# Kernel optimization log

Hardware: AMD Instinct MI355X
Metric: run time of the kernel (lower is better)

The kernel has to match this reference:

```python
import jax, jax.numpy as jnp
import numpy as np

BETA = 0.25
EPS = 1e-10


def setup_inputs() -> dict:
    key = jax.random.key(0)
    k1, k2 = jax.random.split(key)
    z = jax.random.normal(k1, (16, 256, 32, 32), dtype=jnp.float32)
    # Original init: uniform(-1/n_embed, 1/n_embed)
    n_embed, embed_dim = 8192, 256
    codebook = jax.random.uniform(k2, (n_embed, embed_dim), dtype=jnp.float32,
                                  minval=-1.0 / n_embed, maxval=1.0 / n_embed)
    return {"z": z, "codebook": codebook}


def reference(z, codebook):
    B, C, H, W = z.shape
    n_embed = codebook.shape[0]
    zp = jnp.transpose(z, (0, 2, 3, 1))            # (B,H,W,C)
    zf = zp.reshape(-1, C)                          # (N,C)
    # squared L2 distances (N, n_embed)
    d = (jnp.sum(zf * zf, axis=1, keepdims=True)
         + jnp.sum(codebook * codebook, axis=1)
         - 2.0 * zf @ codebook.T)
    idx = jnp.argmin(d, axis=1)                     # (N,)
    zq = codebook[idx].reshape(zp.shape)            # gather == one-hot @ codebook
    commitment_loss = jnp.mean((jax.lax.stop_gradient(zq) - zp) ** 2)
    embedding_loss = jnp.mean((zq - jax.lax.stop_gradient(zp)) ** 2)
    loss = embedding_loss + BETA * commitment_loss
    # straight-through estimator
    zq_st = zp + jax.lax.stop_gradient(zq - zp)
    # perplexity from mean one-hot usage (counts / N)
    counts = jnp.zeros((n_embed,), dtype=zf.dtype).at[idx].add(1.0)
    avg_probs = counts / zf.shape[0]
    perplexity = jnp.exp(-jnp.sum(avg_probs * jnp.log(avg_probs + EPS)))
    zq_out = jnp.transpose(zq_st, (0, 3, 1, 2))     # (B,C,H,W)
    return zq_out, loss, perplexity, idx
```

## Files before the change

kernel.cpp:

```cpp
#include <hip/hip_runtime.h>
#include <math.h>

#define Nrows 16384
#define NE 8192
#define Kdim 256
#define HWsz 1024
#define BETAF 0.25f

typedef __attribute__((ext_vector_type(8))) short bf16x8;
typedef __attribute__((ext_vector_type(16))) float f32x16;
typedef unsigned short u16;

__device__ inline u16 bf16_rne(float x) {
  unsigned int u = __float_as_uint(x);
  return (u16)((u + 0x7FFFu + ((u >> 16) & 1u)) >> 16);
}
__device__ inline float bf16_tof(u16 h) {
  return __uint_as_float(((unsigned int)h) << 16);
}
__device__ inline void gll16(const void* g, void* l) {
  __builtin_amdgcn_global_load_lds(
      (const __attribute__((address_space(1))) unsigned int*)g,
      (__attribute__((address_space(3))) unsigned int*)l, 16, 0, 0);
}

__global__ __launch_bounds__(256) void cc_kernel(const float* __restrict__ cb,
                                                 float* __restrict__ cc) {
  int wave = threadIdx.x >> 6;
  int lane = threadIdx.x & 63;
  int row = blockIdx.x * 4 + wave;
  const float4 v = *(const float4*)(cb + (size_t)row * Kdim + lane * 4);
  float s = v.x * v.x + v.y * v.y + v.z * v.z + v.w * v.w;
  for (int off = 32; off; off >>= 1) s += __shfl_down(s, off);
  if (lane == 0) cc[row] = s;
}

__global__ __launch_bounds__(256) void conv_cb(const float* __restrict__ cb,
                                               u16* __restrict__ Cf) {
  const int g = blockIdx.x * 256 + threadIdx.x;
  const int j = g >> 4, k16 = g & 15;
  const float* src = cb + (size_t)j * Kdim + k16 * 16;
  float f[16];
#pragma unroll
  for (int q = 0; q < 4; ++q) {
    const float4 v = ((const float4*)src)[q];
    f[q * 4 + 0] = v.x; f[q * 4 + 1] = v.y; f[q * 4 + 2] = v.z; f[q * 4 + 3] = v.w;
  }
  u16 h[3][16];
#pragma unroll
  for (int i = 0; i < 16; ++i) {
    const u16 q0 = bf16_rne(f[i]);
    const float r1 = f[i] - bf16_tof(q0);
    const u16 q1 = bf16_rne(r1);
    const float r2 = r1 - bf16_tof(q1);
    h[0][i] = q0; h[1][i] = q1; h[2][i] = bf16_rne(r2);
  }
  const int j32 = j >> 5, li = j & 31;
#pragma unroll
  for (int arr = 0; arr < 3; ++arr) {
#pragma unroll
    for (int kh = 0; kh < 2; ++kh) {
      const size_t off = ((size_t)(j32 * 3 + arr) * 16 + k16) * 512 + (kh * 32 + li) * 8;
      *(int4*)(Cf + off) = *(int4*)&h[arr][kh * 8];
    }
  }
}

__global__ __launch_bounds__(256) void conv_z(const float* __restrict__ z,
                                              u16* __restrict__ Zf,
                                              float* __restrict__ zz) {
  __shared__ float tile[64][68];
  const int t = threadIdx.x;
  const int bid = blockIdx.x;
  const int n0 = bid * 64;
  const int b = bid >> 4;
  const int hw0 = (bid & 15) << 6;
  const float* zb = z + (size_t)b * (Kdim * HWsz) + hw0;
  float zzacc = 0.f;
  const int rr = t >> 2;
  const int kq = (t & 3) * 16;
  for (int kc = 0; kc < 4; ++kc) {
#pragma unroll
    for (int i = 0; i < 16; ++i) {
      const int idx = i * 256 + t;
      const int k = idx >> 6, r = idx & 63;
      tile[r][k] = zb[(size_t)(kc * 64 + k) * HWsz + r];
    }
    __syncthreads();
    if (t < 64) {
      for (int k = 0; k < 64; ++k) {
        const float a = tile[t][k];
        zzacc = fmaf(a, a, zzacc);
      }
    }
    u16 h[3][16];
#pragma unroll
    for (int i = 0; i < 16; ++i) {
      const float fv = tile[rr][kq + i];
      const u16 q0 = bf16_rne(fv);
      const float r1 = fv - bf16_tof(q0);
      const u16 q1 = bf16_rne(r1);
      const float r2 = r1 - bf16_tof(q1);
      h[0][i] = q0; h[1][i] = q1; h[2][i] = bf16_rne(r2);
    }
    const int k16 = kc * 4 + (t & 3);
    const int n32 = bid * 2 + (rr >> 5), li = rr & 31;
#pragma unroll
    for (int arr = 0; arr < 3; ++arr) {
#pragma unroll
      for (int kh = 0; kh < 2; ++kh) {
        const size_t off = ((size_t)(n32 * 3 + arr) * 16 + k16) * 512 + (kh * 32 + li) * 8;
        *(int4*)(Zf + off) = *(int4*)&h[arr][kh * 8];
      }
    }
    __syncthreads();
  }
  if (t < 64) zz[n0 + t] = zzacc;
}

__global__ __launch_bounds__(1024) void vq_gemm(
    const u16* __restrict__ Cf, const u16* __restrict__ Zf,
    const float* __restrict__ cc, const float* __restrict__ zz,
    float* __restrict__ pd, int* __restrict__ pj) {
  __shared__ u16 Zl[49152];
  __shared__ float ccs[1024];
  __shared__ float redD[16][64];
  __shared__ int redJ[16][64];

  const int t = threadIdx.x;
  const int lane = t & 63;
  const int w = __builtin_amdgcn_readfirstlane(t >> 6);
  const int bid = blockIdx.x;
  const int ctg = bid & 7;
  const int rt = bid >> 3;

  ccs[t] = cc[ctg * 1024 + t];

  float zzv[2];
  zzv[0] = zz[rt * 64 + (lane & 31)];
  zzv[1] = zz[rt * 64 + 32 + (lane & 31)];

#pragma unroll
  for (int i = 0; i < 6; ++i) {
    const int g = w * 6 + i;
    const int rg = g & 1, k16 = (g >> 1) & 15, arr = g >> 5;
    gll16(Zf + ((size_t)((rt * 2 + rg) * 3 + arr) * 16 + k16) * 512 + lane * 8,
          &Zl[g * 512]);
  }
  __syncthreads();

  const f32x16 zero16 = {0,0,0,0,0,0,0,0,0,0,0,0,0,0,0,0};
  f32x16 acc[2][2];
  acc[0][0] = zero16; acc[0][1] = zero16; acc[1][0] = zero16; acc[1][1] = zero16;

  for (int ch = 0; ch < 16; ++ch) {
    bf16x8 af[3][2], bfr[3][2];
#pragma unroll
    for (int arr = 0; arr < 3; ++arr) {
#pragma unroll
      for (int x = 0; x < 2; ++x) {
        af[arr][x] = *(const bf16x8*)(
            Cf + ((size_t)((ctg * 32 + w * 2 + x) * 3 + arr) * 16 + ch) * 512 + lane * 8);
        bfr[arr][x] = *(const bf16x8*)&Zl[((arr * 16 + ch) * 2 + x) * 512 + lane * 8];
      }
    }
#define PROD(pa, pb) \
  acc[0][0] = __builtin_amdgcn_mfma_f32_32x32x16_bf16(af[pa][0], bfr[pb][0], acc[0][0], 0, 0, 0); \
  acc[0][1] = __builtin_amdgcn_mfma_f32_32x32x16_bf16(af[pa][0], bfr[pb][1], acc[0][1], 0, 0, 0); \
  acc[1][0] = __builtin_amdgcn_mfma_f32_32x32x16_bf16(af[pa][1], bfr[pb][0], acc[1][0], 0, 0, 0); \
  acc[1][1] = __builtin_amdgcn_mfma_f32_32x32x16_bf16(af[pa][1], bfr[pb][1], acc[1][1], 0, 0, 0);
    PROD(0, 0) PROD(0, 1) PROD(1, 0) PROD(1, 1) PROD(0, 2) PROD(2, 0)
#undef PROD
  }

  float bd[2] = {INFINITY, INFINITY};
  int bj[2] = {0, 0};
#pragma unroll
  for (int ci = 0; ci < 2; ++ci) {
#pragma unroll
    for (int ri = 0; ri < 2; ++ri) {
#pragma unroll
      for (int reg = 0; reg < 16; ++reg) {
        const int cl = w * 64 + ci * 32 +
                       (reg & 3) + ((reg >> 2) * 8) + ((lane >> 5) * 4);
        const float d = (zzv[ri] + ccs[cl]) - 2.0f * acc[ci][ri][reg];
        const int j = ctg * 1024 + cl;
        if (d < bd[ri]) { bd[ri] = d; bj[ri] = j; }
      }
    }
  }

#pragma unroll
  for (int ri = 0; ri < 2; ++ri) {
    const float od = __shfl_xor(bd[ri], 32);
    const int oj = __shfl_xor(bj[ri], 32);
    if (od < bd[ri] || (od == bd[ri] && oj < bj[ri])) { bd[ri] = od; bj[ri] = oj; }
  }
  if (lane < 32) {
    redD[w][lane] = bd[0]; redJ[w][lane] = bj[0];
    redD[w][32 + lane] = bd[1]; redJ[w][32 + lane] = bj[1];
  }
  __syncthreads();
  if (t < 64) {
    float d0 = redD[0][t];
    int j0 = redJ[0][t];
#pragma unroll
    for (int x = 1; x < 16; ++x) {
      const float d = redD[x][t];
      const int j = redJ[x][t];
      if (d < d0 || (d == d0 && j < j0)) { d0 = d; j0 = j; }
    }
    const int n = rt * 64 + t;
    pd[(size_t)ctg * Nrows + n] = d0;
    pj[(size_t)ctg * Nrows + n] = j0;
  }
}

__global__ __launch_bounds__(256) void vq_combine(const float* __restrict__ pd,
                                                  const int* __restrict__ pj,
                                                  int* __restrict__ idx_int,
                                                  float* __restrict__ out_idxf,
                                                  int* __restrict__ counts) {
  const int n = blockIdx.x * 256 + threadIdx.x;
  float d0 = pd[n];
  int j0 = pj[n];
  for (int s = 1; s < 8; ++s) {
    const float d = pd[(size_t)s * Nrows + n];
    const int j = pj[(size_t)s * Nrows + n];
    if (d < d0 || (d == d0 && j < j0)) { d0 = d; j0 = j; }
  }
  idx_int[n] = j0;
  out_idxf[n] = (float)j0;
  atomicAdd(&counts[j0], 1);
}

__global__ __launch_bounds__(256) void vq_gather_loss(
    const float* __restrict__ z, const float* __restrict__ cb,
    const int* __restrict__ idx_int, float* __restrict__ outz,
    float* __restrict__ loss_sum) {
  const int g = blockIdx.x * 256 + threadIdx.x;
  const int hw4 = g & 255;
  const int c = (g >> 8) & 255;
  const int b = g >> 16;
  const int n = b * HWsz + hw4 * 4;
  const float4 zv = *(const float4*)(z + (size_t)g * 4);
  const int4 j4 = *(const int4*)(idx_int + n);
  float4 q;
  q.x = cb[(size_t)j4.x * Kdim + c];
  q.y = cb[(size_t)j4.y * Kdim + c];
  q.z = cb[(size_t)j4.z * Kdim + c];
  q.w = cb[(size_t)j4.w * Kdim + c];
  *(float4*)(outz + (size_t)g * 4) = q;
  float dx = q.x - zv.x, dy = q.y - zv.y, dz = q.z - zv.z, dw = q.w - zv.w;
  float s = dx * dx + dy * dy + dz * dz + dw * dw;
  for (int off = 32; off; off >>= 1) s += __shfl_down(s, off);
  __shared__ float ws4[4];
  if ((threadIdx.x & 63) == 0) ws4[threadIdx.x >> 6] = s;
  __syncthreads();
  if (threadIdx.x == 0) atomicAdd(loss_sum, (ws4[0] + ws4[1]) + (ws4[2] + ws4[3]));
}

__global__ __launch_bounds__(256) void vq_final(const int* __restrict__ counts,
                                                const float* __restrict__ loss_sum,
                                                float* __restrict__ out_sc) {
  float h = 0.f;
  for (int i = threadIdx.x; i < NE; i += 256) {
    float p = (float)counts[i] * (1.0f / 16384.0f);
    h += p * logf(p + 1e-10f);
  }
  for (int off = 32; off; off >>= 1) h += __shfl_down(h, off);
  __shared__ float hs[4];
  if ((threadIdx.x & 63) == 0) hs[threadIdx.x >> 6] = h;
  __syncthreads();
  if (threadIdx.x == 0) {
    float H = (hs[0] + hs[1]) + (hs[2] + hs[3]);
    float m = loss_sum[0] * (1.0f / 4194304.0f);
    out_sc[0] = m + BETAF * m;
    out_sc[1] = expf(-H);
  }
}

extern "C" void kernel_launch(void* const* d_in, const int* in_sizes, int n_in,
                              void* d_out, int out_size, void* d_ws, size_t ws_size,
                              hipStream_t stream) {
  const float* z = (const float*)d_in[0];
  const float* cb = (const float*)d_in[1];
  float* out = (float*)d_out;
  float* out_zq = out;
  float* out_sc = out + 4194304;
  float* out_idx = out + 4194306;

  char* wp = (char*)d_ws;
  u16* Cf = (u16*)wp;           wp += (size_t)NE * Kdim * 2 * 3;
  u16* Zf = (u16*)wp;           wp += (size_t)Nrows * Kdim * 2 * 3;
  float* cc = (float*)wp;       wp += (size_t)NE * 4;
  float* zz = (float*)wp;       wp += (size_t)Nrows * 4;
  float* pd = (float*)wp;       wp += (size_t)8 * Nrows * 4;
  int* pj = (int*)wp;           wp += (size_t)8 * Nrows * 4;
  int* idx_int = (int*)wp;      wp += (size_t)Nrows * 4;
  int* counts = (int*)wp;       wp += (size_t)NE * 4;
  float* loss_sum = (float*)wp; wp += 64;

  hipMemsetAsync(counts, 0, (size_t)NE * 4, stream);
  hipMemsetAsync(loss_sum, 0, 4, stream);

  cc_kernel<<<NE / 4, 256, 0, stream>>>(cb, cc);
  conv_cb<<<NE * 16 / 256, 256, 0, stream>>>(cb, Cf);
  conv_z<<<Nrows / 64, 256, 0, stream>>>(z, Zf, zz);
  vq_gemm<<<2048, 1024, 0, stream>>>(Cf, Zf, cc, zz, pd, pj);
  vq_combine<<<Nrows / 256, 256, 0, stream>>>(pd, pj, idx_int, out_idx, counts);
  vq_gather_loss<<<4096, 256, 0, stream>>>(z, cb, idx_int, out_zq, loss_sum);
  vq_final<<<1, 256, 0, stream>>>(counts, loss_sum, out_sc);
}
```

Baseline: 518.6 us.

## Restructure VQ GEMM into persistent row tiles looping over codebook chunks

The distance GEMM now launches 256 blocks, each owning 1024 z rows (64 per wave held via direct global loads) and looping over 8 codebook tiles of 64 entries staged in LDS, keeping a running argmin in registers. This removes the cross-wave LDS argmin reduction and the per-block reload of z tiles, shifting reuse so codebook tiles are shared in LDS while z fragments stream from global/L2. The codebook is split 16 ways instead of 8, so the combine kernel reads twice as many partial results. Fewer blocks (256) on the 256-CU part and the added per-tile syncs may leave load latency less hidden.

```diff
diff --git a/kernel.cpp b/kernel.cpp
--- a/kernel.cpp
+++ b/kernel.cpp
@@ -5,6 +5,7 @@
 #define NE 8192
 #define Kdim 256
 #define HWsz 1024
+#define NSPL 16
 #define BETAF 0.25f
 
 typedef __attribute__((ext_vector_type(8))) short bf16x8;
@@ -122,70 +123,74 @@
     const u16* __restrict__ Cf, const u16* __restrict__ Zf,
     const float* __restrict__ cc, const float* __restrict__ zz,
     float* __restrict__ pd, int* __restrict__ pj) {
-  __shared__ u16 Zl[49152];
-  __shared__ float ccs[1024];
-  __shared__ float redD[16][64];
-  __shared__ int redJ[16][64];
+  __shared__ u16 Al[49152];
+  __shared__ float ccs[512];
 
   const int t = threadIdx.x;
   const int lane = t & 63;
   const int w = __builtin_amdgcn_readfirstlane(t >> 6);
   const int bid = blockIdx.x;
-  const int ctg = bid & 7;
-  const int rt = bid >> 3;
-
-  ccs[t] = cc[ctg * 1024 + t];
+  const int cg = bid >> 4;
+  const int rg = bid & 15;
+
+  if (t < 512) ccs[t] = cc[cg * 512 + t];
 
   float zzv[2];
-  zzv[0] = zz[rt * 64 + (lane & 31)];
-  zzv[1] = zz[rt * 64 + 32 + (lane & 31)];
-
-#pragma unroll
-  for (int i = 0; i < 6; ++i) {
-    const int g = w * 6 + i;
-    const int rg = g & 1, k16 = (g >> 1) & 15, arr = g >> 5;
-    gll16(Zf + ((size_t)((rt * 2 + rg) * 3 + arr) * 16 + k16) * 512 + lane * 8,
-          &Zl[g * 512]);
-  }
-  __syncthreads();
-
+  zzv[0] = zz[rg * 1024 + w * 64 + (lane & 31)];
+  zzv[1] = zz[rg * 1024 + w * 64 + 32 + (lane & 31)];
+
+  float bd[2] = {INFINITY, INFINITY};
+  int bj[2] = {0, 0};
   const f32x16 zero16 = {0,0,0,0,0,0,0,0,0,0,0,0,0,0,0,0};
-  f32x16 acc[2][2];
-  acc[0][0] = zero16; acc[0][1] = zero16; acc[1][0] = zero16; acc[1][1] = zero16;
-
-  for (int ch = 0; ch < 16; ++ch) {
-    bf16x8 af[3][2], bfr[3][2];
-#pragma unroll
-    for (int arr = 0; arr < 3; ++arr) {
-#pragma unroll
-      for (int x = 0; x < 2; ++x) {
-        af[arr][x] = *(const bf16x8*)(
-            Cf + ((size_t)((ctg * 32 + w * 2 + x) * 3 + arr) * 16 + ch) * 512 + lane * 8);
-        bfr[arr][x] = *(const bf16x8*)&Zl[((arr * 16 + ch) * 2 + x) * 512 + lane * 8];
+
+  for (int ct = 0; ct < 8; ++ct) {
+    __syncthreads();
+#pragma unroll
+    for (int i = 0; i < 6; ++i) {
+      const int g = w * 6 + i;
+      const int ja = g >> 4;
+      const int jx = ja / 3, arr = ja % 3;
+      const int k16 = g & 15;
+      gll16(Cf + ((size_t)((cg * 16 + ct * 2 + jx) * 3 + arr) * 16 + k16) * 512 + lane * 8,
+            &Al[g * 512]);
+    }
+    __syncthreads();
+
+    f32x16 acc[2][2];
+    acc[0][0] = zero16; acc[0][1] = zero16; acc[1][0] = zero16; acc[1][1] = zero16;
+
+    for (int ch = 0; ch < 16; ++ch) {
+      bf16x8 af[3][2], bfr[3][2];
+#pragma unroll
+      for (int arr = 0; arr < 3; ++arr) {
+#pragma unroll
+        for (int x = 0; x < 2; ++x) {
+          af[arr][x] = *(const bf16x8*)&Al[((x * 3 + arr) * 16 + ch) * 512 + lane * 8];
+          bfr[arr][x] = *(const bf16x8*)(
+              Zf + ((size_t)((rg * 32 + w * 2 + x) * 3 + arr) * 16 + ch) * 512 + lane * 8);
+        }
       }
-    }
 #define PROD(pa, pb) \
   acc[0][0] = __builtin_amdgcn_mfma_f32_32x32x16_bf16(af[pa][0], bfr[pb][0], acc[0][0], 0, 0, 0); \
   acc[0][1] = __builtin_amdgcn_mfma_f32_32x32x16_bf16(af[pa][0], bfr[pb][1], acc[0][1], 0, 0, 0); \
   acc[1][0] = __builtin_amdgcn_mfma_f32_32x32x16_bf16(af[pa][1], bfr[pb][0], acc[1][0], 0, 0, 0); \
   acc[1][1] = __builtin_amdgcn_mfma_f32_32x32x16_bf16(af[pa][1], bfr[pb][1], acc[1][1], 0, 0, 0);
-    PROD(0, 0) PROD(0, 1) PROD(1, 0) PROD(1, 1) PROD(0, 2) PROD(2, 0)
+      PROD(0, 0) PROD(0, 1) PROD(1, 0) PROD(1, 1) PROD(0, 2) PROD(2, 0)
 #undef PROD
-  }
-
-  float bd[2] = {INFINITY, INFINITY};
-  int bj[2] = {0, 0};
-#pragma unroll
-  for (int ci = 0; ci < 2; ++ci) {
-#pragma unroll
-    for (int ri = 0; ri < 2; ++ri) {
-#pragma unroll
-      for (int reg = 0; reg < 16; ++reg) {
-        const int cl = w * 64 + ci * 32 +
-                       (reg & 3) + ((reg >> 2) * 8) + ((lane >> 5) * 4);
-        const float d = (zzv[ri] + ccs[cl]) - 2.0f * acc[ci][ri][reg];
-        const int j = ctg * 1024 + cl;
-        if (d < bd[ri]) { bd[ri] = d; bj[ri] = j; }
+    }
+
+#pragma unroll
+    for (int ci = 0; ci < 2; ++ci) {
+#pragma unroll
+      for (int ri = 0; ri < 2; ++ri) {
+#pragma unroll
+        for (int reg = 0; reg < 16; ++reg) {
+          const int cl = ct * 64 + ci * 32 +
+                         (reg & 3) + ((reg >> 2) * 8) + ((lane >> 5) * 4);
+          const float d = (zzv[ri] + ccs[cl]) - 2.0f * acc[ci][ri][reg];
+          const int j = cg * 512 + cl;
+          if (d < bd[ri]) { bd[ri] = d; bj[ri] = j; }
+        }
       }
     }
   }
@@ -197,22 +202,12 @@
     if (od < bd[ri] || (od == bd[ri] && oj < bj[ri])) { bd[ri] = od; bj[ri] = oj; }
   }
   if (lane < 32) {
-    redD[w][lane] = bd[0]; redJ[w][lane] = bj[0];
-    redD[w][32 + lane] = bd[1]; redJ[w][32 + lane] = bj[1];
-  }
-  __syncthreads();
-  if (t < 64) {
-    float d0 = redD[0][t];
-    int j0 = redJ[0][t];
-#pragma unroll
-    for (int x = 1; x < 16; ++x) {
-      const float d = redD[x][t];
-      const int j = redJ[x][t];
-      if (d < d0 || (d == d0 && j < j0)) { d0 = d; j0 = j; }
-    }
-    const int n = rt * 64 + t;
-    pd[(size_t)ctg * Nrows + n] = d0;
-    pj[(size_t)ctg * Nrows + n] = j0;
+#pragma unroll
+    for (int ri = 0; ri < 2; ++ri) {
+      const int n = rg * 1024 + w * 64 + ri * 32 + lane;
+      pd[(size_t)cg * Nrows + n] = bd[ri];
+      pj[(size_t)cg * Nrows + n] = bj[ri];
+    }
   }
 }
 
@@ -224,7 +219,7 @@
   const int n = blockIdx.x * 256 + threadIdx.x;
   float d0 = pd[n];
   int j0 = pj[n];
-  for (int s = 1; s < 8; ++s) {
+  for (int s = 1; s < NSPL; ++s) {
     const float d = pd[(size_t)s * Nrows + n];
     const int j = pj[(size_t)s * Nrows + n];
     if (d < d0 || (d == d0 && j < j0)) { d0 = d; j0 = j; }
@@ -295,8 +290,8 @@
   u16* Zf = (u16*)wp;           wp += (size_t)Nrows * Kdim * 2 * 3;
   float* cc = (float*)wp;       wp += (size_t)NE * 4;
   float* zz = (float*)wp;       wp += (size_t)Nrows * 4;
-  float* pd = (float*)wp;       wp += (size_t)8 * Nrows * 4;
-  int* pj = (int*)wp;           wp += (size_t)8 * Nrows * 4;
+  float* pd = (float*)wp;       wp += (size_t)NSPL * Nrows * 4;
+  int* pj = (int*)wp;           wp += (size_t)NSPL * Nrows * 4;
   int* idx_int = (int*)wp;      wp += (size_t)Nrows * 4;
   int* counts = (int*)wp;       wp += (size_t)NE * 4;
   float* loss_sum = (float*)wp; wp += 64;
@@ -307,7 +302,7 @@
   cc_kernel<<<NE / 4, 256, 0, stream>>>(cb, cc);
   conv_cb<<<NE * 16 / 256, 256, 0, stream>>>(cb, Cf);
   conv_z<<<Nrows / 64, 256, 0, stream>>>(z, Zf, zz);
-  vq_gemm<<<2048, 1024, 0, stream>>>(Cf, Zf, cc, zz, pd, pj);
+  vq_gemm<<<256, 1024, 0, stream>>>(Cf, Zf, cc, zz, pd, pj);
   vq_combine<<<Nrows / 256, 256, 0, stream>>>(pd, pj, idx_int, out_idx, counts);
   vq_gather_loss<<<4096, 256, 0, stream>>>(z, cb, idx_int, out_zq, loss_sum);
   vq_final<<<1, 256, 0, stream>>>(counts, loss_sum, out_sc);
```

Result: slower. 1.071 ms (+106.5%).
